# Kernel optimization log

Hardware: AMD Instinct MI355X
Metric: run time of the kernel (lower is better)

The kernel has to match this reference:

```python
import jax, jax.numpy as jnp
import numpy as np
import math

V, L, H, D, T_MAX, FF = 50257, 12, 12, 768, 1024, 3072
B, T = 2, 1024
HD = D // H


def layernorm(x, g, b, eps=1e-5):
    m = x.mean(-1, keepdims=True)
    v = ((x - m) ** 2).mean(-1, keepdims=True)
    return (x - m) / jnp.sqrt(v + eps) * g + b


def mgelu(x):
    # note: module uses 0.047715 (not the standard 0.044715)
    return 0.5 * x * (1.0 + jnp.tanh(math.sqrt(2.0 / math.pi) * (x + 0.047715 * x ** 3)))


def setup_inputs() -> dict:
    key = jax.random.key(0)
    ks = jax.random.split(key, 16)
    s = 0.02
    sr = 0.02 * (2 * L) ** -0.5  # residual-projection init per GPT2 paper
    inp = {
        "idx": jax.random.randint(ks[0], (B, T), 0, V),
        "targets": jax.random.randint(ks[1], (B, T), 0, V),
        "wte": jax.random.normal(ks[2], (V, D), jnp.float32) * s,
        "wpe": jax.random.normal(ks[3], (T_MAX, D), jnp.float32) * s,
        "ln1_g": jnp.ones((L, D), jnp.float32),
        "ln1_b": jnp.zeros((L, D), jnp.float32),
        "qkv_w": jax.random.normal(ks[4], (L, D, 3 * D), jnp.float32) * s,
        "qkv_b": jnp.zeros((L, 3 * D), jnp.float32),
        "po_w": jax.random.normal(ks[5], (L, D, D), jnp.float32) * sr,
        "po_b": jnp.zeros((L, D), jnp.float32),
        "ln2_g": jnp.ones((L, D), jnp.float32),
        "ln2_b": jnp.zeros((L, D), jnp.float32),
        "fc_w": jax.random.normal(ks[6], (L, D, FF), jnp.float32) * s,
        "fc_b": jnp.zeros((L, FF), jnp.float32),
        "pr_w": jax.random.normal(ks[7], (L, FF, D), jnp.float32) * sr,
        "pr_b": jnp.zeros((L, D), jnp.float32),
        "lnf_g": jnp.ones((D,), jnp.float32),
        "lnf_b": jnp.zeros((D,), jnp.float32),
        "lm_w": jax.random.normal(ks[8], (D, V), jnp.float32) * s,
    }
    return inp


def gpt_forward(idx, targets, wte, wpe, ln1_g, ln1_b, qkv_w, qkv_b, po_w, po_b,
                ln2_g, ln2_b, fc_w, fc_b, pr_w, pr_b, lnf_g, lnf_b, lm_w):
    Bt, Tt = idx.shape
    x = wte[idx] + wpe[:Tt]  # [B,T,D]
    causal = jnp.tril(jnp.ones((Tt, Tt), bool))
    scale = 1.0 / math.sqrt(HD)

    def block(x, p):
        g1, b1, wq, bq, wo, bo, g2, b2, wf, bf, wp, bp = p
        h = layernorm(x, g1, b1)
        qkv = h @ wq + bq  # [B,T,3D]
        q, k, v = jnp.split(qkv, 3, axis=-1)
        q = q.reshape(Bt, Tt, H, HD)
        k = k.reshape(Bt, Tt, H, HD)
        v = v.reshape(Bt, Tt, H, HD)
        att = jnp.einsum('bqhd,bkhd->bhqk', q, k) * scale
        att = jnp.where(causal, att, -jnp.inf)
        att = jax.nn.softmax(att, axis=-1)  # dropout = identity (eval)
        y = jnp.einsum('bhqk,bkhd->bqhd', att, v).reshape(Bt, Tt, D)
        x = x + y @ wo + bo
        h2 = layernorm(x, g2, b2)
        x = x + mgelu(h2 @ wf + bf) @ wp + bp
        return x, None

    x, _ = jax.lax.scan(block, x, (ln1_g, ln1_b, qkv_w, qkv_b, po_w, po_b,
                                   ln2_g, ln2_b, fc_w, fc_b, pr_w, pr_b))
    x = layernorm(x, lnf_g, lnf_b)
    logits = x @ lm_w  # [B,T,V]

    logp = jax.nn.log_softmax(logits, axis=-1)
    valid = targets >= 0  # ignore_index=-1
    tgt = jnp.where(valid, targets, 0)
    nll = -jnp.take_along_axis(logp, tgt[..., None], axis=-1)[..., 0]
    loss = (nll * valid).sum() / valid.sum()
    return logits, loss


def reference(idx, targets, wte, wpe, ln1_g, ln1_b, qkv_w, qkv_b, po_w, po_b,
              ln2_g, ln2_b, fc_w, fc_b, pr_w, pr_b, lnf_g, lnf_b, lm_w):
    return gpt_forward(idx, targets, wte, wpe, ln1_g, ln1_b, qkv_w, qkv_b, po_w, po_b,
                       ln2_g, ln2_b, fc_w, fc_b, pr_w, pr_b, lnf_g, lnf_b, lm_w)
```

## Files before the change

### kernel.cpp

```cpp
#include <hip/hip_runtime.h>
#include <hip/hip_bf16.h>
#include <math.h>

#define VOC 50257
#define NL 12
#define NH 12
#define DM 768
#define FF 3072
#define BB 2
#define TT 1024
#define MR (BB*TT)

typedef __attribute__((ext_vector_type(8))) short bf16x8;
typedef __attribute__((ext_vector_type(4))) float f32x4;

__device__ __forceinline__ float mgelu_f(float x) {
    return 0.5f*x*(1.f + tanhf(0.7978845608028654f*(x + 0.047715f*x*x*x)));
}

__device__ __forceinline__ unsigned short f2bf(float f) {
    __hip_bfloat16 h = __float2bfloat16(f);
    return *reinterpret_cast<unsigned short*>(&h);
}

__device__ __forceinline__ int xcd_work(int bid, int total) {
    int xcd = bid & 7;
    int seq = bid >> 3;
    int q = total >> 3, r = total & 7;
    int base = (xcd < r) ? xcd*(q+1) : r + xcd*q;
    return base + seq;
}

__global__ void embed_kernel(const int* __restrict__ idx, const float* __restrict__ wte,
                             const float* __restrict__ wpe, float* __restrict__ x) {
    int row = blockIdx.x;
    int t = row % TT;
    int tok = idx[row];
    for (int d = threadIdx.x; d < DM; d += blockDim.x)
        x[(size_t)row*DM + d] = wte[(size_t)tok*DM + d] + wpe[(size_t)t*DM + d];
}

__global__ __launch_bounds__(256) void ln_kernel(const float* __restrict__ x,
                          const float* __restrict__ g,
                          const float* __restrict__ b, __hip_bfloat16* __restrict__ out) {
    int row = blockIdx.x*4 + (threadIdx.x >> 6);
    int lane = threadIdx.x & 63;
    const float* xr = x + (size_t)row*DM;
    float vals[DM/64];
    float s = 0.f;
    #pragma unroll
    for (int i = 0; i < DM/64; i++) { vals[i] = xr[lane + i*64]; s += vals[i]; }
    #pragma unroll
    for (int off = 32; off > 0; off >>= 1) s += __shfl_xor(s, off);
    float mean = s * (1.0f/DM);
    float vs = 0.f;
    #pragma unroll
    for (int i = 0; i < DM/64; i++) { float d = vals[i]-mean; vs += d*d; }
    #pragma unroll
    for (int off = 32; off > 0; off >>= 1) vs += __shfl_xor(vs, off);
    float rstd = rsqrtf(vs * (1.0f/DM) + 1e-5f);
    #pragma unroll
    for (int i = 0; i < DM/64; i++) {
        int d = lane + i*64;
        out[(size_t)row*DM + d] = __float2bfloat16((vals[i]-mean)*rstd*g[d] + b[d]);
    }
}

struct TJob { const float* in; __hip_bfloat16* out; int R, C, cx, tile0; };

__device__ __forceinline__ void trans_one(const TJob& j, int t) {
    __shared__ float tile[32][33];
    int bx = t % j.cx, by = t / j.cx;
    int c0 = bx*32, r0 = by*32;
    int tx = threadIdx.x, ty = threadIdx.y;
    #pragma unroll
    for (int i = ty; i < 32; i += 8) {
        int r = r0 + i, c = c0 + tx;
        tile[i][tx] = (r < j.R && c < j.C) ? j.in[(size_t)r*j.C + c] : 0.f;
    }
    __syncthreads();
    #pragma unroll
    for (int i = ty; i < 32; i += 8) {
        int c = c0 + i, r = r0 + tx;
        if (c < j.C && r < j.R) j.out[(size_t)c*j.R + r] = __float2bfloat16(tile[tx][i]);
    }
}

__global__ void trans4_kernel(TJob j0, TJob j1, TJob j2, TJob j3) {
    int t = blockIdx.x;
    if (t >= j3.tile0)      trans_one(j3, t - j3.tile0);
    else if (t >= j2.tile0) trans_one(j2, t - j2.tile0);
    else if (t >= j1.tile0) trans_one(j1, t - j1.tile0);
    else                    trans_one(j0, t);
}

__global__ void trans1_kernel(TJob j0) { trans_one(j0, blockIdx.x); }

template<int MODE, int HALFM>
__global__ __launch_bounds__(256) void mfma_gemm_kernel(
        const __hip_bfloat16* __restrict__ A,
        const __hip_bfloat16* __restrict__ Wt,
        const float* __restrict__ bias,
        const float* __restrict__ res,
        void* __restrict__ Cout,
        __hip_bfloat16* __restrict__ vt,
        int M, int N, int K) {
    constexpr int BM = HALFM ? 64 : 128;
    constexpr int NF = HALFM ? 2 : 4;
    __shared__ __align__(16) char As[BM*64];
    __shared__ __align__(16) char Bs[8192];
    int tid = threadIdx.x;
    int lane = tid & 63, wid = tid >> 6;
    int kq = lane >> 4, lr = lane & 15;

    int nby = M / BM;
    int work = xcd_work(blockIdx.x, gridDim.x);
    int by = work % nby;
    int bx = work / nby;
    int m0 = by * BM, n0 = bx * 128;

    int wm = HALFM ? 0 : (wid >> 1);
    int wn = HALFM ? wid : (wid & 1);
    int colbase = HALFM ? wn*32 : wn*64;

    f32x4 acc[4][NF] = {};

    for (int k0 = 0; k0 < K; k0 += 32) {
        if constexpr (HALFM) {
            const __hip_bfloat16* ga = A + (size_t)(m0 + lane)*K + k0 + wid*8;
            __builtin_amdgcn_global_load_lds(
                (const __attribute__((address_space(1))) void*)ga,
                (__attribute__((address_space(3))) void*)(As + wid*1024), 16, 0, 0);
            #pragma unroll
            for (int t = 0; t < 2; t++) {
                int lx = wid + t*4;
                int r  = (lx & 1)*64 + lane;
                int kk = (lx >> 1)*8;
                int nr = n0 + r; if (nr > N-1) nr = N-1;
                const __hip_bfloat16* gb = Wt + (size_t)nr*K + k0 + kk;
                __builtin_amdgcn_global_load_lds(
                    (const __attribute__((address_space(1))) void*)gb,
                    (__attribute__((address_space(3))) void*)(Bs + lx*1024), 16, 0, 0);
            }
        } else {
            #pragma unroll
            for (int t = 0; t < 2; t++) {
                int lx = wid + t*4;
                int r  = (lx & 1)*64 + lane;
                int kk = (lx >> 1)*8;
                const __hip_bfloat16* ga = A + (size_t)(m0 + r)*K + k0 + kk;
                __builtin_amdgcn_global_load_lds(
                    (const __attribute__((address_space(1))) void*)ga,
                    (__attribute__((address_space(3))) void*)(As + lx*1024), 16, 0, 0);
                int nr = n0 + r; if (nr > N-1) nr = N-1;
                const __hip_bfloat16* gb = Wt + (size_t)nr*K + k0 + kk;
                __builtin_amdgcn_global_load_lds(
                    (const __attribute__((address_space(1))) void*)gb,
                    (__attribute__((address_space(3))) void*)(Bs + lx*1024), 16, 0, 0);
            }
        }
        __syncthreads();

        bf16x8 afrag[4], bfrag[NF];
        #pragma unroll
        for (int m = 0; m < 4; m++)
            afrag[m] = *(const bf16x8*)(As + kq*(BM*16) + (wm*64 + m*16 + lr)*16);
        #pragma unroll
        for (int n = 0; n < NF; n++)
            bfrag[n] = *(const bf16x8*)(Bs + kq*2048 + (colbase + n*16 + lr)*16);
        #pragma unroll
        for (int m = 0; m < 4; m++)
            #pragma unroll
            for (int n = 0; n < NF; n++)
                acc[m][n] = __builtin_amdgcn_mfma_f32_16x16x32_bf16(afrag[m], bfrag[n], acc[m][n], 0, 0, 0);
        __syncthreads();
    }

    #pragma unroll
    for (int m = 0; m < 4; m++) {
        #pragma unroll
        for (int n = 0; n < NF; n++) {
            int col = n0 + colbase + n*16 + lr;
            if (col >= N) continue;
            float bv = (MODE == 0) ? 0.f : bias[col];
            #pragma unroll
            for (int j = 0; j < 4; j++) {
                int row = m0 + wm*64 + m*16 + kq*4 + j;
                float v = acc[m][n][j] + bv;
                size_t o = (size_t)row*N + col;
                if (MODE == 0) {
                    ((float*)Cout)[o] = v;
                } else if (MODE == 1) {
                    __hip_bfloat16 bvv = __float2bfloat16(v);
                    ((__hip_bfloat16*)Cout)[o] = bvv;
                    if (col >= 2*DM) {
                        int hh = (col - 2*DM) >> 6, dd = (col - 2*DM) & 63;
                        int bb = row >> 10, tt = row & 1023;
                        vt[(((size_t)bb*NH + hh)*64 + dd)*TT + tt] = bvv;
                    }
                } else if (MODE == 2) {
                    ((float*)Cout)[o] = v + res[o];
                } else {
                    ((__hip_bfloat16*)Cout)[o] = __float2bfloat16(mgelu_f(v));
                }
            }
        }
    }
}

__global__ __launch_bounds__(256) void mfma_attn_kernel(const __hip_bfloat16* __restrict__ qkv,
                                                        const __hip_bfloat16* __restrict__ vt,
                                                        __hip_bfloat16* __restrict__ y) {
    __shared__ __align__(16) char K_lds[8192];
    __shared__ __align__(16) char VT_lds[8192];
    __shared__ __align__(16) char P_lds[4][2048];

    int work = xcd_work(blockIdx.x, BB*NH*16);
    int qt = 15 - (work & 15);
    int bh = work >> 4;
    int h  = bh % NH;
    int b  = bh / NH;
    int tid = threadIdx.x;
    int lane = tid & 63, w = tid >> 6;
    int lr = lane & 15, kq = lane >> 4;
    int q0 = qt * 64;

    int sr = lane >> 3;
    int scb = (lane & 7) * 16;

    int qrow = q0 + w*16 + lr;
    const __hip_bfloat16* qp = qkv + (size_t)(b*TT + qrow)*3*DM + h*64;
    bf16x8 qfrag[2];
    qfrag[0] = *(const bf16x8*)(qp + kq*8);
    qfrag[1] = *(const bf16x8*)(qp + 32 + kq*8);

    f32x4 oacc[4] = {};
    float m_run = -INFINITY, l_run = 0.f;
    const float scale = 0.125f;

    const char* kbase  = (const char*)qkv + ((size_t)b*TT*3*DM + DM + h*64)*2;
    const char* vtbase = (const char*)vt + ((size_t)(b*NH + h)*64)*TT*2;

    for (int kt = 0; kt <= qt; ++kt) {
        int kv0 = kt*64;
        #pragma unroll
        for (int t = 0; t < 2; t++) {
            int lx = w + t*4;
            int r = lx*8 + sr;
            int cbs = scb ^ ((r & 7) << 4);
            const char* gk = kbase + (size_t)(kv0 + r)*3*DM*2 + cbs;
            __builtin_amdgcn_global_load_lds(
                (const __attribute__((address_space(1))) void*)gk,
                (__attribute__((address_space(3))) void*)(K_lds + lx*1024), 16, 0, 0);
            const char* gv = vtbase + (size_t)r*TT*2 + kv0*2 + cbs;
            __builtin_amdgcn_global_load_lds(
                (const __attribute__((address_space(1))) void*)gv,
                (__attribute__((address_space(3))) void*)(VT_lds + lx*1024), 16, 0, 0);
        }
        __syncthreads();

        f32x4 st[4] = {};
        #pragma unroll
        for (int t = 0; t < 4; ++t) {
            #pragma unroll
            for (int ks = 0; ks < 2; ++ks) {
                int row = t*16 + lr;
                bf16x8 kf = *(const bf16x8*)(K_lds + row*128 + ((ks*64 + kq*16) ^ ((lr&7)<<4)));
                st[t] = __builtin_amdgcn_mfma_f32_16x16x32_bf16(kf, qfrag[ks], st[t], 0,0,0);
            }
        }

        float sv[4][4];
        bool diag = (kt == qt);
        float pmax = -INFINITY;
        #pragma unroll
        for (int t = 0; t < 4; ++t)
            #pragma unroll
            for (int jj = 0; jj < 4; ++jj) {
                float s = st[t][jj] * scale;
                if (diag && (t*16 + kq*4 + jj > w*16 + lr)) s = -INFINITY;
                sv[t][jj] = s;
                pmax = fmaxf(pmax, s);
            }
        pmax = fmaxf(pmax, __shfl_xor(pmax, 16));
        pmax = fmaxf(pmax, __shfl_xor(pmax, 32));
        float m_new = fmaxf(m_run, pmax);
        float corr = __expf(m_run - m_new);
        float rsum = 0.f;
        #pragma unroll
        for (int t = 0; t < 4; ++t)
            #pragma unroll
            for (int jj = 0; jj < 4; ++jj) {
                float p = __expf(sv[t][jj] - m_new);
                sv[t][jj] = p;
                rsum += p;
            }
        rsum += __shfl_xor(rsum, 16);
        rsum += __shfl_xor(rsum, 32);
        l_run = l_run * corr + rsum;
        m_run = m_new;

        #pragma unroll
        for (int jj = 0; jj < 4; ++jj) {
            float c = __shfl(corr, kq*20 + jj);
            #pragma unroll
            for (int nt = 0; nt < 4; ++nt) oacc[nt][jj] *= c;
        }

        #pragma unroll
        for (int t = 0; t < 4; ++t) {
            unsigned pk0 = (unsigned)f2bf(sv[t][0]) | ((unsigned)f2bf(sv[t][1]) << 16);
            unsigned pk1 = (unsigned)f2bf(sv[t][2]) | ((unsigned)f2bf(sv[t][3]) << 16);
            unsigned off = ((unsigned)(lr*128 + t*32 + kq*8)) ^ (((unsigned)lr&7u)<<4);
            *(uint2*)(P_lds[w] + off) = make_uint2(pk0, pk1);
        }

        #pragma unroll
        for (int ks = 0; ks < 2; ++ks) {
            bf16x8 pa = *(const bf16x8*)(P_lds[w] +
                ((unsigned)(lr*128 + ((ks*64 + kq*16) ^ ((lr&7)<<4)))));
            #pragma unroll
            for (int nt = 0; nt < 4; ++nt) {
                int row = nt*16 + lr;
                bf16x8 vf = *(const bf16x8*)(VT_lds + row*128 + ((ks*64 + kq*16) ^ ((lr&7)<<4)));
                oacc[nt] = __builtin_amdgcn_mfma_f32_16x16x32_bf16(pa, vf, oacc[nt], 0,0,0);
            }
        }
        __syncthreads();
    }

    #pragma unroll
    for (int jj = 0; jj < 4; ++jj) {
        float li = __shfl(l_run, kq*20 + jj);
        int qg = q0 + w*16 + kq*4 + jj;
        #pragma unroll
        for (int nt = 0; nt < 4; ++nt)
            y[(size_t)(b*TT + qg)*DM + h*64 + nt*16 + lr] =
                __float2bfloat16(oacc[nt][jj] / li);
    }
}

__global__ void zero_acc_kernel(float* p) { p[threadIdx.x] = 0.f; }

__global__ __launch_bounds__(256) void loss_kernel(const float* __restrict__ logits,
                                                   const int* __restrict__ targets,
                                                   float* __restrict__ acc) {
    int row = blockIdx.x;
    int tid = threadIdx.x;
    __shared__ float red[256];
    const float* lr = logits + (size_t)row * VOC;
    float mx = -INFINITY;
    for (int c = tid; c < VOC; c += 256) mx = fmaxf(mx, lr[c]);
    red[tid] = mx; __syncthreads();
    for (int off = 128; off > 0; off >>= 1) {
        if (tid < off) red[tid] = fmaxf(red[tid], red[tid+off]);
        __syncthreads();
    }
    mx = red[0]; __syncthreads();
    float se = 0.f;
    for (int c = tid; c < VOC; c += 256) se += expf(lr[c] - mx);
    red[tid] = se; __syncthreads();
    for (int off = 128; off > 0; off >>= 1) {
        if (tid < off) red[tid] += red[tid+off];
        __syncthreads();
    }
    if (tid == 0) {
        int tgt = targets[row];
        if (tgt >= 0) {
            float lse = logf(red[0]) + mx;
            atomicAdd(&acc[0], lse - lr[tgt]);
            atomicAdd(&acc[1], 1.f);
        }
    }
}

__global__ void loss_final_kernel(const float* acc, float* out) {
    out[0] = acc[0] / acc[1];
}

static inline TJob mkjob(const float* in, __hip_bfloat16* out, int R, int C, int tile0) {
    TJob j; j.in = in; j.out = out; j.R = R; j.C = C;
    j.cx = (C + 31)/32; j.tile0 = tile0;
    return j;
}

extern "C" void kernel_launch(void* const* d_in, const int* in_sizes, int n_in,
                              void* d_out, int out_size, void* d_ws, size_t ws_size,
                              hipStream_t stream) {
    const int*   idx     = (const int*)  d_in[0];
    const int*   targets = (const int*)  d_in[1];
    const float* wte     = (const float*)d_in[2];
    const float* wpe     = (const float*)d_in[3];
    const float* ln1_g   = (const float*)d_in[4];
    const float* ln1_b   = (const float*)d_in[5];
    const float* qkv_w   = (const float*)d_in[6];
    const float* qkv_b   = (const float*)d_in[7];
    const float* po_w    = (const float*)d_in[8];
    const float* po_b    = (const float*)d_in[9];
    const float* ln2_g   = (const float*)d_in[10];
    const float* ln2_b   = (const float*)d_in[11];
    const float* fc_w    = (const float*)d_in[12];
    const float* fc_b    = (const float*)d_in[13];
    const float* pr_w    = (const float*)d_in[14];
    const float* pr_b    = (const float*)d_in[15];
    const float* lnf_g   = (const float*)d_in[16];
    const float* lnf_b   = (const float*)d_in[17];
    const float* lm_w    = (const float*)d_in[18];

    float* logits = (float*)d_out;

    char* p = (char*)d_ws;
    float* x = (float*)p;                 p += (size_t)MR*DM*4;
    __hip_bfloat16* h    = (__hip_bfloat16*)p; p += (size_t)MR*DM*2;
    __hip_bfloat16* qkvb = (__hip_bfloat16*)p; p += (size_t)MR*3*DM*2;
    __hip_bfloat16* yb   = (__hip_bfloat16*)p; p += (size_t)MR*DM*2;
    __hip_bfloat16* fb   = (__hip_bfloat16*)p; p += (size_t)MR*FF*2;
    __hip_bfloat16* vtb  = (__hip_bfloat16*)p; p += (size_t)BB*NH*64*TT*2;
    __hip_bfloat16* lm_wt  = (__hip_bfloat16*)p; p += (size_t)VOC*DM*2;
    __hip_bfloat16* qkv_wt = (__hip_bfloat16*)p; p += (size_t)3*DM*DM*2;
    __hip_bfloat16* po_wt  = (__hip_bfloat16*)p; p += (size_t)DM*DM*2;
    __hip_bfloat16* fc_wt  = (__hip_bfloat16*)p; p += (size_t)FF*DM*2;
    __hip_bfloat16* pr_wt  = (__hip_bfloat16*)p; p += (size_t)DM*FF*2;
    float* lacc = (float*)p;

    dim3 tpb(32, 8);

    embed_kernel<<<MR, 256, 0, stream>>>(idx, wte, wpe, x);

    {
        TJob j = mkjob(lm_w, lm_wt, DM, VOC, 0);
        int tiles = j.cx * ((DM+31)/32);
        trans1_kernel<<<tiles, tpb, 0, stream>>>(j);
    }

    for (int l = 0; l < NL; l++) {
        TJob j0 = mkjob(qkv_w + (size_t)l*DM*3*DM, qkv_wt, DM, 3*DM, 0);
        int t1 = j0.cx * 24;
        TJob j1 = mkjob(po_w + (size_t)l*DM*DM, po_wt, DM, DM, t1);
        int t2 = t1 + j1.cx * 24;
        TJob j2 = mkjob(fc_w + (size_t)l*DM*FF, fc_wt, DM, FF, t2);
        int t3 = t2 + j2.cx * 24;
        TJob j3 = mkjob(pr_w + (size_t)l*FF*DM, pr_wt, FF, DM, t3);
        int tot = t3 + j3.cx * 96;
        trans4_kernel<<<tot, tpb, 0, stream>>>(j0, j1, j2, j3);

        ln_kernel<<<MR/4, 256, 0, stream>>>(x, ln1_g + l*DM, ln1_b + l*DM, h);
        mfma_gemm_kernel<1,0><<<(3*DM/128)*(MR/128), 256, 0, stream>>>(
            h, qkv_wt, qkv_b + (size_t)l*3*DM, nullptr, qkvb, vtb, MR, 3*DM, DM);
        mfma_attn_kernel<<<BB*NH*(TT/64), 256, 0, stream>>>(qkvb, vtb, yb);
        mfma_gemm_kernel<2,1><<<(DM/128)*(MR/64), 256, 0, stream>>>(
            yb, po_wt, po_b + (size_t)l*DM, x, x, nullptr, MR, DM, DM);
        ln_kernel<<<MR/4, 256, 0, stream>>>(x, ln2_g + l*DM, ln2_b + l*DM, h);
        mfma_gemm_kernel<3,0><<<(FF/128)*(MR/128), 256, 0, stream>>>(
            h, fc_wt, fc_b + (size_t)l*FF, nullptr, fb, nullptr, MR, FF, DM);
        mfma_gemm_kernel<2,1><<<(DM/128)*(MR/64), 256, 0, stream>>>(
            fb, pr_wt, pr_b + (size_t)l*DM, x, x, nullptr, MR, DM, FF);
    }

    ln_kernel<<<MR/4, 256, 0, stream>>>(x, lnf_g, lnf_b, h);
    mfma_gemm_kernel<0,0><<<((VOC+127)/128)*(MR/128), 256, 0, stream>>>(
        h, lm_wt, nullptr, nullptr, logits, nullptr, MR, VOC, DM);

    zero_acc_kernel<<<1, 2, 0, stream>>>(lacc);
    loss_kernel<<<MR, 256, 0, stream>>>(logits, targets, lacc);
    loss_final_kernel<<<1, 1, 0, stream>>>(lacc, logits + (size_t)MR*VOC);
}
```

Before: 3.436 ms.

## Double-buffer LDS tiles in GEMM and attention; single-pass online-softmax loss

```diff
diff --git a/kernel.cpp b/kernel.cpp
--- a/kernel.cpp
+++ b/kernel.cpp
@@ -22,6 +22,10 @@
     __hip_bfloat16 h = __float2bfloat16(f);
     return *reinterpret_cast<unsigned short*>(&h);
 }
+
+#define GLDS(gptr, lptr) __builtin_amdgcn_global_load_lds( \
+    (const __attribute__((address_space(1))) void*)(gptr), \
+    (__attribute__((address_space(3))) void*)(lptr), 16, 0, 0)
 
 __device__ __forceinline__ int xcd_work(int bid, int total) {
     int xcd = bid & 7;
@@ -107,8 +111,8 @@
         int M, int N, int K) {
     constexpr int BM = HALFM ? 64 : 128;
     constexpr int NF = HALFM ? 2 : 4;
-    __shared__ __align__(16) char As[BM*64];
-    __shared__ __align__(16) char Bs[8192];
+    __shared__ __align__(16) char As[2][BM*64];
+    __shared__ __align__(16) char Bs[2][8192];
     int tid = threadIdx.x;
     int lane = tid & 63, wid = tid >> 6;
     int kq = lane >> 4, lr = lane & 15;
@@ -125,22 +129,16 @@
 
     f32x4 acc[4][NF] = {};
 
-    for (int k0 = 0; k0 < K; k0 += 32) {
+    auto STAGE = [&](int buf, int k0) {
         if constexpr (HALFM) {
-            const __hip_bfloat16* ga = A + (size_t)(m0 + lane)*K + k0 + wid*8;
-            __builtin_amdgcn_global_load_lds(
-                (const __attribute__((address_space(1))) void*)ga,
-                (__attribute__((address_space(3))) void*)(As + wid*1024), 16, 0, 0);
+            GLDS(A + (size_t)(m0 + lane)*K + k0 + wid*8, As[buf] + wid*1024);
             #pragma unroll
             for (int t = 0; t < 2; t++) {
                 int lx = wid + t*4;
                 int r  = (lx & 1)*64 + lane;
                 int kk = (lx >> 1)*8;
                 int nr = n0 + r; if (nr > N-1) nr = N-1;
-                const __hip_bfloat16* gb = Wt + (size_t)nr*K + k0 + kk;
-                __builtin_amdgcn_global_load_lds(
-                    (const __attribute__((address_space(1))) void*)gb,
-                    (__attribute__((address_space(3))) void*)(Bs + lx*1024), 16, 0, 0);
+                GLDS(Wt + (size_t)nr*K + k0 + kk, Bs[buf] + lx*1024);
             }
         } else {
             #pragma unroll
@@ -148,26 +146,27 @@
                 int lx = wid + t*4;
                 int r  = (lx & 1)*64 + lane;
                 int kk = (lx >> 1)*8;
-                const __hip_bfloat16* ga = A + (size_t)(m0 + r)*K + k0 + kk;
-                __builtin_amdgcn_global_load_lds(
-                    (const __attribute__((address_space(1))) void*)ga,
-                    (__attribute__((address_space(3))) void*)(As + lx*1024), 16, 0, 0);
+                GLDS(A + (size_t)(m0 + r)*K + k0 + kk, As[buf] + lx*1024);
                 int nr = n0 + r; if (nr > N-1) nr = N-1;
-                const __hip_bfloat16* gb = Wt + (size_t)nr*K + k0 + kk;
-                __builtin_amdgcn_global_load_lds(
-                    (const __attribute__((address_space(1))) void*)gb,
-                    (__attribute__((address_space(3))) void*)(Bs + lx*1024), 16, 0, 0);
-            }
-        }
-        __syncthreads();
+                GLDS(Wt + (size_t)nr*K + k0 + kk, Bs[buf] + lx*1024);
+            }
+        }
+    };
+
+    int nk = K >> 5;
+    STAGE(0, 0);
+    __syncthreads();
+    for (int ki = 0; ki < nk; ++ki) {
+        int cur = ki & 1;
+        if (ki + 1 < nk) STAGE(cur ^ 1, (ki+1)*32);
 
         bf16x8 afrag[4], bfrag[NF];
         #pragma unroll
         for (int m = 0; m < 4; m++)
-            afrag[m] = *(const bf16x8*)(As + kq*(BM*16) + (wm*64 + m*16 + lr)*16);
+            afrag[m] = *(const bf16x8*)(As[cur] + kq*(BM*16) + (wm*64 + m*16 + lr)*16);
         #pragma unroll
         for (int n = 0; n < NF; n++)
-            bfrag[n] = *(const bf16x8*)(Bs + kq*2048 + (colbase + n*16 + lr)*16);
+            bfrag[n] = *(const bf16x8*)(Bs[cur] + kq*2048 + (colbase + n*16 + lr)*16);
         #pragma unroll
         for (int m = 0; m < 4; m++)
             #pragma unroll
@@ -211,8 +210,8 @@
 __global__ __launch_bounds__(256) void mfma_attn_kernel(const __hip_bfloat16* __restrict__ qkv,
                                                         const __hip_bfloat16* __restrict__ vt,
                                                         __hip_bfloat16* __restrict__ y) {
-    __shared__ __align__(16) char K_lds[8192];
-    __shared__ __align__(16) char VT_lds[8192];
+    __shared__ __align__(16) char K_lds[2][8192];
+    __shared__ __align__(16) char VT_lds[2][8192];
     __shared__ __align__(16) char P_lds[4][2048];
 
     int work = xcd_work(blockIdx.x, BB*NH*16);
@@ -241,23 +240,23 @@
     const char* kbase  = (const char*)qkv + ((size_t)b*TT*3*DM + DM + h*64)*2;
     const char* vtbase = (const char*)vt + ((size_t)(b*NH + h)*64)*TT*2;
 
-    for (int kt = 0; kt <= qt; ++kt) {
+    auto STAGE = [&](int buf, int kt) {
         int kv0 = kt*64;
         #pragma unroll
         for (int t = 0; t < 2; t++) {
             int lx = w + t*4;
             int r = lx*8 + sr;
             int cbs = scb ^ ((r & 7) << 4);
-            const char* gk = kbase + (size_t)(kv0 + r)*3*DM*2 + cbs;
-            __builtin_amdgcn_global_load_lds(
-                (const __attribute__((address_space(1))) void*)gk,
-                (__attribute__((address_space(3))) void*)(K_lds + lx*1024), 16, 0, 0);
-            const char* gv = vtbase + (size_t)r*TT*2 + kv0*2 + cbs;
-            __builtin_amdgcn_global_load_lds(
-                (const __attribute__((address_space(1))) void*)gv,
-                (__attribute__((address_space(3))) void*)(VT_lds + lx*1024), 16, 0, 0);
-        }
-        __syncthreads();
+            GLDS(kbase + (size_t)(kv0 + r)*3*DM*2 + cbs, K_lds[buf] + lx*1024);
+            GLDS(vtbase + (size_t)r*TT*2 + kv0*2 + cbs, VT_lds[buf] + lx*1024);
+        }
+    };
+
+    STAGE(0, 0);
+    __syncthreads();
+    for (int kt = 0; kt <= qt; ++kt) {
+        int cur = kt & 1;
+        if (kt < qt) STAGE(cur ^ 1, kt + 1);
 
         f32x4 st[4] = {};
         #pragma unroll
@@ -265,7 +264,7 @@
             #pragma unroll
             for (int ks = 0; ks < 2; ++ks) {
                 int row = t*16 + lr;
-                bf16x8 kf = *(const bf16x8*)(K_lds + row*128 + ((ks*64 + kq*16) ^ ((lr&7)<<4)));
+                bf16x8 kf = *(const bf16x8*)(K_lds[cur] + row*128 + ((ks*64 + kq*16) ^ ((lr&7)<<4)));
                 st[t] = __builtin_amdgcn_mfma_f32_16x16x32_bf16(kf, qfrag[ks], st[t], 0,0,0);
             }
         }
@@ -322,7 +321,7 @@
             #pragma unroll
             for (int nt = 0; nt < 4; ++nt) {
                 int row = nt*16 + lr;
-                bf16x8 vf = *(const bf16x8*)(VT_lds + row*128 + ((ks*64 + kq*16) ^ ((lr&7)<<4)));
+                bf16x8 vf = *(const bf16x8*)(VT_lds[cur] + row*128 + ((ks*64 + kq*16) ^ ((lr&7)<<4)));
                 oacc[nt] = __builtin_amdgcn_mfma_f32_16x16x32_bf16(pa, vf, oacc[nt], 0,0,0);
             }
         }
@@ -347,27 +346,34 @@
                                                    float* __restrict__ acc) {
     int row = blockIdx.x;
     int tid = threadIdx.x;
-    __shared__ float red[256];
     const float* lr = logits + (size_t)row * VOC;
-    float mx = -INFINITY;
-    for (int c = tid; c < VOC; c += 256) mx = fmaxf(mx, lr[c]);
-    red[tid] = mx; __syncthreads();
+    float m = -INFINITY, s = 0.f;
+    for (int c4 = tid; c4 < 12564; c4 += 256) {
+        float4 v = ((const float4*)lr)[c4];
+        float vm = fmaxf(fmaxf(v.x, v.y), fmaxf(v.z, v.w));
+        if (vm > m) { s *= __expf(m - vm); m = vm; }
+        s += __expf(v.x - m) + __expf(v.y - m) + __expf(v.z - m) + __expf(v.w - m);
+    }
+    if (tid == 0) {
+        float v = lr[VOC - 1];
+        if (v > m) { s *= __expf(m - v); m = v; }
+        s += __expf(v - m);
+    }
+    __shared__ float rm[256], rs[256];
+    rm[tid] = m; rs[tid] = s; __syncthreads();
     for (int off = 128; off > 0; off >>= 1) {
-        if (tid < off) red[tid] = fmaxf(red[tid], red[tid+off]);
-        __syncthreads();
-    }
-    mx = red[0]; __syncthreads();
-    float se = 0.f;
-    for (int c = tid; c < VOC; c += 256) se += expf(lr[c] - mx);
-    red[tid] = se; __syncthreads();
-    for (int off = 128; off > 0; off >>= 1) {
-        if (tid < off) red[tid] += red[tid+off];
+        if (tid < off) {
+            float m2 = rm[tid+off], s2 = rs[tid+off];
+            float M = fmaxf(rm[tid], m2);
+            rs[tid] = rs[tid]*__expf(rm[tid]-M) + s2*__expf(m2-M);
+            rm[tid] = M;
+        }
         __syncthreads();
     }
     if (tid == 0) {
         int tgt = targets[row];
         if (tgt >= 0) {
-            float lse = logf(red[0]) + mx;
+            float lse = logf(rs[0]) + rm[0];
             atomicAdd(&acc[0], lse - lr[tgt]);
             atomicAdd(&acc[1], 1.f);
         }
```

After: 3.291 ms. -4.2%, faster.
